# Optimization experiments

Measured on AMD Instinct MI355X. Metric: run time of the kernel, lower is better.

## Reference

```python
import jax, jax.numpy as jnp
import numpy as np

KH, KW = 3, 3
PAD = 1
IN_C = 3
OUT_C = 16
QUBITS = 5            # max(ceil(log2(3*3*3))=5, ceil(log2(16))=4)
QDEPTH = 1
DIM = 2 ** QUBITS     # 32 amplitudes per patch
FEAT = KH * KW * IN_C # 27 unfolded features per patch
EPS = 0.001           # self.almost_zero


def setup_inputs() -> dict:
    key = jax.random.key(0)
    k1, k2 = jax.random.split(key)
    x = jax.random.normal(k1, (8, 3, 224, 224), dtype=jnp.float32)
    # StronglyEntanglingLayer rotation angles (depth, qubits, 3) in [0, 2pi)
    weights = jax.random.uniform(k2, (QDEPTH, QUBITS, 3), dtype=jnp.float32,
                                 minval=0.0, maxval=2.0 * np.pi)
    return {"x": x, "weights": weights}


def _rot(phi, theta, omega):
    # PennyLane/qandle Rot(phi, theta, omega) = RZ(omega) RY(theta) RZ(phi)
    c = jnp.cos(theta * 0.5).astype(jnp.complex64)
    s = jnp.sin(theta * 0.5).astype(jnp.complex64)
    em = jnp.exp(-0.5j * (phi + omega))   # e^{-i(phi+omega)/2}
    ep = jnp.exp(0.5j * (phi + omega))
    epm = jnp.exp(0.5j * (phi - omega))
    emp = jnp.exp(-0.5j * (phi - omega))
    row0 = jnp.stack([em * c, -epm * s])
    row1 = jnp.stack([emp * s, ep * c])
    return jnp.stack([row0, row1])  # (2, 2) complex64


def _apply_1q(psi, U, q):
    # psi: (N, 2, 2, 2, 2, 2); apply 2x2 unitary on qubit q
    psi = jnp.moveaxis(psi, 1 + q, -1)
    psi = psi @ U.T  # new_a = sum_b U[a,b] psi[..., b]
    return jnp.moveaxis(psi, -1, 1 + q)


def _cnot(psi, c, t):
    # control qubit c, target qubit t: flip target where control == 1
    p0, p1 = jnp.split(psi, 2, axis=1 + c)
    p1 = jnp.flip(p1, axis=1 + t)
    return jnp.concatenate([p0, p1], axis=1 + c)


def reference(x, weights):
    b, cin, h, w = x.shape
    # --- Unfold (kernel 3x3, pad 1, stride 1) -> (b, c*kh*kw, h*w), torch layout ---
    xp = jnp.pad(x, ((0, 0), (0, 0), (PAD, PAD), (PAD, PAD)))
    cols = jnp.stack([xp[:, :, i:i + h, j:j + w]
                      for i in range(KH) for j in range(KW)], axis=2)  # (b, c, 9, h, w)
    v = cols.reshape(b, FEAT, h * w)
    # rearrange 'batch channel feat -> (batch feat) channel'
    v = jnp.transpose(v, (0, 2, 1)).reshape(b * h * w, FEAT) + EPS
    # --- AmplitudeEmbedding: pad with 0 to 2^qubits, L2-normalize ---
    v = jnp.pad(v, ((0, 0), (0, DIM - FEAT)))
    psi = (v / jnp.linalg.norm(v, axis=1, keepdims=True)).astype(jnp.complex64)
    psi = psi.reshape((b * h * w,) + (2,) * QUBITS)
    # --- StronglyEntanglingLayer: Rot on each qubit, then CNOT ring ---
    for d in range(QDEPTH):
        for q in range(QUBITS):
            U = _rot(weights[d, q, 0], weights[d, q, 1], weights[d, q, 2])
            psi = _apply_1q(psi, U, q)
        for q in range(QUBITS):
            psi = _cnot(psi, q, (q + 1) % QUBITS)
    # --- MeasureJointProbability: |amplitude|^2 over all basis states ---
    psi = psi.reshape(b * h * w, DIM)
    probs = psi.real ** 2 + psi.imag ** 2
    # --- post-process: keep first out_channels, scale ---
    out = probs[:, :OUT_C] * (OUT_C / 2.0)
    # rearrange '(batch h w) channel -> batch channel h w'
    out = jnp.transpose(out.reshape(b, h * w, OUT_C), (0, 2, 1))
    return out.reshape(b, OUT_C, h, w)
```

## Files before the change

kernel.cpp:

```cpp
#include <hip/hip_runtime.h>

#define H 224
#define W 224
#define HW (H * W)
#define OUTC 16
#define FEAT 27
#define EPSV 0.001f
#define PH 226
#define PW 228
#define PLANE (PH * PW)
#define NPAD (24 * PLANE)
#define PAD_BLOCKS ((NPAD + 255) / 256)

typedef float f4 __attribute__((ext_vector_type(4)));
typedef float f2 __attribute__((ext_vector_type(2)));

__global__ __launch_bounds__(256) void prep(const float* __restrict__ x,
                                            const float* __restrict__ w,
                                            float* __restrict__ pbuf,
                                            float2* __restrict__ M) {
    if (blockIdx.x == gridDim.x - 1) {
        __shared__ float sre[32][33];
        __shared__ float sim_[32][33];
        const int j = threadIdx.x;
        if (j >= 32) return;

        for (int i = 0; i < 32; ++i) {
            sre[j][i] = (i == j) ? 1.0f : 0.0f;
            sim_[j][i] = 0.0f;
        }
        for (int q = 0; q < 5; ++q) {
            float phi = w[q * 3 + 0];
            float th  = w[q * 3 + 1];
            float om  = w[q * 3 + 2];
            float ch = cosf(0.5f * th), sh = sinf(0.5f * th);
            float al = 0.5f * (phi + om), be = 0.5f * (phi - om);
            float ca = cosf(al), sa = sinf(al);
            float cb = cosf(be), sb = sinf(be);
            float u00r =  ca * ch, u00i = -sa * ch;
            float u01r = -cb * sh, u01i = -sb * sh;
            float u10r =  cb * sh, u10i = -sb * sh;
            float u11r =  ca * ch, u11i =  sa * ch;
            int m = 1 << (4 - q);
            for (int i = 0; i < 32; ++i) {
                if (i & m) continue;
                float a0r = sre[j][i],     a0i = sim_[j][i];
                float a1r = sre[j][i | m], a1i = sim_[j][i | m];
                sre[j][i]      = u00r * a0r - u00i * a0i + u01r * a1r - u01i * a1i;
                sim_[j][i]     = u00r * a0i + u00i * a0r + u01r * a1i + u01i * a1r;
                sre[j][i | m]  = u10r * a0r - u10i * a0i + u11r * a1r - u11i * a1i;
                sim_[j][i | m] = u10r * a0i + u10i * a0r + u11r * a1i + u11i * a1r;
            }
        }
        for (int q = 0; q < 5; ++q) {
            int mc = 1 << (4 - q);
            int mt = 1 << (4 - ((q + 1) % 5));
            for (int i = 0; i < 32; ++i) {
                if ((i & mc) && !(i & mt)) {
                    int i2 = i | mt;
                    float tr = sre[j][i]; sre[j][i] = sre[j][i2]; sre[j][i2] = tr;
                    float ti = sim_[j][i]; sim_[j][i] = sim_[j][i2]; sim_[j][i2] = ti;
                }
            }
        }
        if (j < FEAT) {
            for (int k = 0; k < OUTC; ++k)
                M[k * FEAT + j] = make_float2(sre[j][k], sim_[j][k]);
        }
        return;
    }

    int i = blockIdx.x * 256 + threadIdx.x;
    if (i >= NPAD) return;
    int px = i % PW;
    int rest = i / PW;
    int py = rest % PH;
    int cc = rest / PH;
    float val = EPSV;
    int ix = px - 1, iy = py - 1;
    if (ix >= 0 && ix < W && iy >= 0 && iy < H)
        val = x[cc * HW + iy * W + ix] + EPSV;
    pbuf[i] = val;
}

__global__ __launch_bounds__(256) void qconv(const float* __restrict__ pbuf,
                                             const float2* __restrict__ M,
                                             float* __restrict__ out) {
    __shared__ float2 Ms[OUTC * FEAT];
    const int tid = threadIdx.x;
    Ms[tid] = M[tid];
    if (tid < OUTC * FEAT - 256) Ms[256 + tid] = M[256 + tid];
    __syncthreads();

    const int khalf = blockIdx.x & 1;
    const int g = (blockIdx.x >> 1) * 256 + tid;
    const int x4 = (g % 56) * 4;
    int rest = g / 56;
    const int y = rest % H;
    const int b = rest / H;

    float r[3][3][6];
    #pragma unroll
    for (int c = 0; c < 3; ++c) {
        #pragma unroll
        for (int ki = 0; ki < 3; ++ki) {
            const float* rp = pbuf + ((b * 3 + c) * PLANE) + (y + ki) * PW + x4;
            f4 a = *(const f4*)rp;
            f2 t = *(const f2*)(rp + 4);
            r[c][ki][0] = a.x; r[c][ki][1] = a.y; r[c][ki][2] = a.z; r[c][ki][3] = a.w;
            r[c][ki][4] = t.x; r[c][ki][5] = t.y;
        }
    }

    float scale[4];
    #pragma unroll
    for (int p = 0; p < 4; ++p) {
        float n2 = 0.0f;
        #pragma unroll
        for (int c = 0; c < 3; ++c)
            #pragma unroll
            for (int ki = 0; ki < 3; ++ki)
                #pragma unroll
                for (int kj = 0; kj < 3; ++kj) {
                    float t = r[c][ki][p + kj];
                    n2 = fmaf(t, t, n2);
                }
        scale[p] = 8.0f / n2;
    }

    float* ob = out + ((size_t)b * OUTC + khalf * 8) * HW + y * W + x4;
    #pragma unroll
    for (int kk = 0; kk < 8; ++kk) {
        float re[4] = {0, 0, 0, 0}, im[4] = {0, 0, 0, 0};
        #pragma unroll
        for (int f = 0; f < FEAT; ++f) {
            float2 m = Ms[(khalf * 8 + kk) * FEAT + f];
            const int c = f / 9, rr = (f % 9) / 3, kj = f % 3;
            #pragma unroll
            for (int p = 0; p < 4; ++p) {
                float t = r[c][rr][p + kj];
                re[p] = fmaf(m.x, t, re[p]);
                im[p] = fmaf(m.y, t, im[p]);
            }
        }
        f4 o;
        o.x = (re[0] * re[0] + im[0] * im[0]) * scale[0];
        o.y = (re[1] * re[1] + im[1] * im[1]) * scale[1];
        o.z = (re[2] * re[2] + im[2] * im[2]) * scale[2];
        o.w = (re[3] * re[3] + im[3] * im[3]) * scale[3];
        *(f4*)(ob + kk * HW) = o;
    }
}

extern "C" void kernel_launch(void* const* d_in, const int* in_sizes, int n_in,
                              void* d_out, int out_size, void* d_ws, size_t ws_size,
                              hipStream_t stream) {
    const float* x = (const float*)d_in[0];
    const float* w = (const float*)d_in[1];
    float* out = (float*)d_out;

    float2* M = (float2*)d_ws;
    float* pbuf = (float*)((char*)d_ws + 4096);

    prep<<<PAD_BLOCKS + 1, 256, 0, stream>>>(x, w, pbuf, M);

    qconv<<<784, 256, 0, stream>>>(pbuf, M, out);
}
```

Measured before the change: 91.08 us.

## Fuse padding prep and unitary build into single qconv kernel

Drops the separate prep kernel, which wrote a padded, eps-shifted copy of the input to workspace and built the 16x27 complex matrix in one block. Each qconv block now rebuilds the unitary columns it needs in shared memory, with the gate work spread across all 256 threads, and applies the CNOT ring as an index permutation. Input rows are read straight from x with boundary masks plus scalar loads for the left and right halo. This removes a kernel launch and a full padded-buffer round trip through memory, at the cost of repeating the small unitary computation and its barriers in every block.

```diff
diff --git a/kernel.cpp b/kernel.cpp
--- a/kernel.cpp
+++ b/kernel.cpp
@@ -6,109 +6,89 @@
 #define OUTC 16
 #define FEAT 27
 #define EPSV 0.001f
-#define PH 226
-#define PW 228
-#define PLANE (PH * PW)
-#define NPAD (24 * PLANE)
-#define PAD_BLOCKS ((NPAD + 255) / 256)
 
 typedef float f4 __attribute__((ext_vector_type(4)));
-typedef float f2 __attribute__((ext_vector_type(2)));
 
-__global__ __launch_bounds__(256) void prep(const float* __restrict__ x,
-                                            const float* __restrict__ w,
-                                            float* __restrict__ pbuf,
-                                            float2* __restrict__ M) {
-    if (blockIdx.x == gridDim.x - 1) {
-        __shared__ float sre[32][33];
-        __shared__ float sim_[32][33];
-        const int j = threadIdx.x;
-        if (j >= 32) return;
+__global__ __launch_bounds__(256) void qconv_fused(const float* __restrict__ x,
+                                                   const float* __restrict__ w,
+                                                   float* __restrict__ out) {
+    __shared__ float2 amp[32][32];
+    __shared__ float2 Ms[8 * FEAT];
 
-        for (int i = 0; i < 32; ++i) {
-            sre[j][i] = (i == j) ? 1.0f : 0.0f;
-            sim_[j][i] = 0.0f;
+    const int tid = threadIdx.x;
+    const int khalf = blockIdx.x & 1;
+
+    #pragma unroll
+    for (int e = tid; e < 1024; e += 256) {
+        int j = e >> 5, i = e & 31;
+        amp[j][i] = make_float2((i == j) ? 1.0f : 0.0f, 0.0f);
+    }
+    __syncthreads();
+
+    #pragma unroll
+    for (int q = 0; q < 5; ++q) {
+        float phi = w[q * 3 + 0], th = w[q * 3 + 1], om = w[q * 3 + 2];
+        float sh, ch; sincosf(0.5f * th, &sh, &ch);
+        float sa, ca; sincosf(0.5f * (phi + om), &sa, &ca);
+        float sb, cb; sincosf(0.5f * (phi - om), &sb, &cb);
+        float u00r =  ca * ch, u00i = -sa * ch;
+        float u01r = -cb * sh, u01i = -sb * sh;
+        float u10r =  cb * sh, u10i = -sb * sh;
+        float u11r =  ca * ch, u11i =  sa * ch;
+        const int m = 1 << (4 - q);
+        #pragma unroll
+        for (int rep = 0; rep < 2; ++rep) {
+            int pidx = tid + rep * 256;
+            int j = pidx >> 4, pp = pidx & 15;
+            int i0 = ((pp & ~(m - 1)) << 1) | (pp & (m - 1));
+            int i1 = i0 | m;
+            float2 a0 = amp[j][i0], a1 = amp[j][i1];
+            float2 n0, n1;
+            n0.x = u00r * a0.x - u00i * a0.y + u01r * a1.x - u01i * a1.y;
+            n0.y = u00r * a0.y + u00i * a0.x + u01r * a1.y + u01i * a1.x;
+            n1.x = u10r * a0.x - u10i * a0.y + u11r * a1.x - u11i * a1.y;
+            n1.y = u10r * a0.y + u10i * a0.x + u11r * a1.y + u11i * a1.x;
+            amp[j][i0] = n0; amp[j][i1] = n1;
         }
-        for (int q = 0; q < 5; ++q) {
-            float phi = w[q * 3 + 0];
-            float th  = w[q * 3 + 1];
-            float om  = w[q * 3 + 2];
-            float ch = cosf(0.5f * th), sh = sinf(0.5f * th);
-            float al = 0.5f * (phi + om), be = 0.5f * (phi - om);
-            float ca = cosf(al), sa = sinf(al);
-            float cb = cosf(be), sb = sinf(be);
-            float u00r =  ca * ch, u00i = -sa * ch;
-            float u01r = -cb * sh, u01i = -sb * sh;
-            float u10r =  cb * sh, u10i = -sb * sh;
-            float u11r =  ca * ch, u11i =  sa * ch;
-            int m = 1 << (4 - q);
-            for (int i = 0; i < 32; ++i) {
-                if (i & m) continue;
-                float a0r = sre[j][i],     a0i = sim_[j][i];
-                float a1r = sre[j][i | m], a1i = sim_[j][i | m];
-                sre[j][i]      = u00r * a0r - u00i * a0i + u01r * a1r - u01i * a1i;
-                sim_[j][i]     = u00r * a0i + u00i * a0r + u01r * a1i + u01i * a1r;
-                sre[j][i | m]  = u10r * a0r - u10i * a0i + u11r * a1r - u11i * a1i;
-                sim_[j][i | m] = u10r * a0i + u10i * a0r + u11r * a1i + u11i * a1r;
-            }
-        }
-        for (int q = 0; q < 5; ++q) {
-            int mc = 1 << (4 - q);
-            int mt = 1 << (4 - ((q + 1) % 5));
-            for (int i = 0; i < 32; ++i) {
-                if ((i & mc) && !(i & mt)) {
-                    int i2 = i | mt;
-                    float tr = sre[j][i]; sre[j][i] = sre[j][i2]; sre[j][i2] = tr;
-                    float ti = sim_[j][i]; sim_[j][i] = sim_[j][i2]; sim_[j][i2] = ti;
-                }
-            }
-        }
-        if (j < FEAT) {
-            for (int k = 0; k < OUTC; ++k)
-                M[k * FEAT + j] = make_float2(sre[j][k], sim_[j][k]);
-        }
-        return;
+        __syncthreads();
     }
 
-    int i = blockIdx.x * 256 + threadIdx.x;
-    if (i >= NPAD) return;
-    int px = i % PW;
-    int rest = i / PW;
-    int py = rest % PH;
-    int cc = rest / PH;
-    float val = EPSV;
-    int ix = px - 1, iy = py - 1;
-    if (ix >= 0 && ix < W && iy >= 0 && iy < H)
-        val = x[cc * HW + iy * W + ix] + EPSV;
-    pbuf[i] = val;
-}
-
-__global__ __launch_bounds__(256) void qconv(const float* __restrict__ pbuf,
-                                             const float2* __restrict__ M,
-                                             float* __restrict__ out) {
-    __shared__ float2 Ms[OUTC * FEAT];
-    const int tid = threadIdx.x;
-    Ms[tid] = M[tid];
-    if (tid < OUTC * FEAT - 256) Ms[256 + tid] = M[256 + tid];
+    for (int e = tid; e < 8 * FEAT; e += 256) {
+        int kk = e / FEAT, j = e % FEAT;
+        int i = khalf * 8 + kk;
+        #pragma unroll
+        for (int q = 4; q >= 0; --q) {
+            int pc = 4 - q, pt = 4 - ((q + 1) % 5);
+            i ^= ((i >> pc) & 1) << pt;
+        }
+        Ms[e] = amp[j][i];
+    }
     __syncthreads();
 
-    const int khalf = blockIdx.x & 1;
     const int g = (blockIdx.x >> 1) * 256 + tid;
     const int x4 = (g % 56) * 4;
     int rest = g / 56;
     const int y = rest % H;
     const int b = rest / H;
+    const float* xb = x + b * 3 * HW;
 
     float r[3][3][6];
     #pragma unroll
     for (int c = 0; c < 3; ++c) {
         #pragma unroll
         for (int ki = 0; ki < 3; ++ki) {
-            const float* rp = pbuf + ((b * 3 + c) * PLANE) + (y + ki) * PW + x4;
-            f4 a = *(const f4*)rp;
-            f2 t = *(const f2*)(rp + 4);
-            r[c][ki][0] = a.x; r[c][ki][1] = a.y; r[c][ki][2] = a.z; r[c][ki][3] = a.w;
-            r[c][ki][4] = t.x; r[c][ki][5] = t.y;
+            int iy = y + ki - 1;
+            bool rowok = (iy >= 0) && (iy < H);
+            const float* rp = xb + c * HW + iy * W + x4;
+            f4 mid = rowok ? *(const f4*)rp : (f4){0.f, 0.f, 0.f, 0.f};
+            float left  = (rowok && x4 > 0)   ? rp[-1] : 0.0f;
+            float right = (rowok && x4 < 220) ? rp[4]  : 0.0f;
+            r[c][ki][0] = left  + EPSV;
+            r[c][ki][1] = mid.x + EPSV;
+            r[c][ki][2] = mid.y + EPSV;
+            r[c][ki][3] = mid.z + EPSV;
+            r[c][ki][4] = mid.w + EPSV;
+            r[c][ki][5] = right + EPSV;
         }
     }
 
@@ -134,7 +114,7 @@
         float re[4] = {0, 0, 0, 0}, im[4] = {0, 0, 0, 0};
         #pragma unroll
         for (int f = 0; f < FEAT; ++f) {
-            float2 m = Ms[(khalf * 8 + kk) * FEAT + f];
+            float2 m = Ms[kk * FEAT + f];
             const int c = f / 9, rr = (f % 9) / 3, kj = f % 3;
             #pragma unroll
             for (int p = 0; p < 4; ++p) {
@@ -158,11 +138,7 @@
     const float* x = (const float*)d_in[0];
     const float* w = (const float*)d_in[1];
     float* out = (float*)d_out;
+    (void)d_ws; (void)ws_size;
 
-    float2* M = (float2*)d_ws;
-    float* pbuf = (float*)((char*)d_ws + 4096);
-
-    prep<<<PAD_BLOCKS + 1, 256, 0, stream>>>(x, w, pbuf, M);
-
-    qconv<<<784, 256, 0, stream>>>(pbuf, M, out);
+    qconv_fused<<<784, 256, 0, stream>>>(x, w, out);
 }
```

New measurement: 81.23 us. -10.8%, faster.
